# Kernel optimization log

Measured on AMD Instinct MI355X. Metric: run time of the kernel, lower is better.

The kernel has to match this reference:

```python
import jax, jax.numpy as jnp
import numpy as np

N = 50000            # nodes (cells)
E_RAND = 1_600_000   # random edges; self loops appended -> E = E_RAND + N
DIMS = [(512, 384), (384, 256), (256, 128)]  # (in, hidden) per encoder stage
OUT = 128


def setup_inputs() -> dict:
    key = jax.random.key(0)
    ks = jax.random.split(key, 16)
    features = jax.random.normal(ks[0], (N, DIMS[0][0]), dtype=jnp.float32)
    src = jax.random.randint(ks[1], (E_RAND,), 0, N, dtype=jnp.int32)
    dst = jax.random.randint(ks[2], (E_RAND,), 0, N, dtype=jnp.int32)
    loops = jnp.arange(N, dtype=jnp.int32)  # dgl.add_self_loop
    src = jnp.concatenate([src, loops])
    dst = jnp.concatenate([dst, loops])
    inp = {"features": features, "src": src, "dst": dst}
    i = 3
    for s, (din, dout) in enumerate(DIMS):
        inp[f"sage_w{s}"] = jax.random.normal(ks[i], (dout, din), jnp.float32) / np.sqrt(din); i += 1
        inp[f"sage_b{s}"] = jnp.zeros((dout,), jnp.float32)
        inp[f"gc_w{s}"] = jax.random.normal(ks[i], (dout, dout), jnp.float32) / np.sqrt(dout); i += 1
        inp[f"gc_b{s}"] = jnp.zeros((dout,), jnp.float32)
    inp["fc_w"] = jax.random.normal(ks[i], (OUT, DIMS[-1][1]), jnp.float32) / np.sqrt(DIMS[-1][1])
    inp["fc_b"] = jnp.zeros((OUT,), jnp.float32)
    return inp


def reference(features, src, dst,
              sage_w0, sage_b0, gc_w0, gc_b0,
              sage_w1, sage_b1, gc_w1, gc_b1,
              sage_w2, sage_b2, gc_w2, gc_b2,
              fc_w, fc_b):
    ones = jnp.ones((src.shape[0],), jnp.float32)
    in_deg = jax.ops.segment_sum(ones, dst, num_segments=N)
    out_deg = jax.ops.segment_sum(ones, src, num_segments=N)
    # GraphConv norm='both' scalers (clamp degree to >=1, as DGL does)
    inv_src = jnp.where(out_deg > 0, out_deg, 1.0) ** -0.5  # [N]
    inv_dst = jnp.where(in_deg > 0, in_deg, 1.0) ** -0.5    # [N]
    sage_den = (in_deg + 1.0)[:, None]                      # SAGE 'gcn' denominator

    def sage_gcn(h, w, b):
        # DGL SAGEConv aggregator_type='gcn': (sum_neigh + self)/(in_deg+1) -> fc_neigh
        agg = jax.ops.segment_sum(h[src], dst, num_segments=N)
        return ((agg + h) / sage_den) @ w.T + b

    def graph_conv(h, w, b):
        # DGL GraphConv norm='both': D_out^{-1/2} -> sum aggregate -> D_in^{-1/2} -> W
        hn = h * inv_src[:, None]
        agg = jax.ops.segment_sum(hn[src], dst, num_segments=N)
        return (agg * inv_dst[:, None]) @ w.T + b

    params = [(sage_w0, sage_b0, gc_w0, gc_b0),
              (sage_w1, sage_b1, gc_w1, gc_b1),
              (sage_w2, sage_b2, gc_w2, gc_b2)]
    h = features
    for sw, sb, gw, gb in params:
        h = jax.nn.relu(sage_gcn(h, sw, sb))
        h = jax.nn.relu(graph_conv(h, gw, gb))
    return h @ fc_w.T + fc_b
```

## Files before the change

kernel.cpp:

```cpp
#include <hip/hip_runtime.h>
#include <cstddef>
#include <cstdint>


typedef _Float16 h8 __attribute__((ext_vector_type(8)));
typedef _Float16 h4 __attribute__((ext_vector_type(4)));
typedef float f32x4 __attribute__((ext_vector_type(4)));

#define HB 64
#define NCH 256


__global__ __launch_bounds__(1024) void histo_dst_kernel(
    const int* __restrict__ dst, uint32_t* __restrict__ H,
    int* __restrict__ ord, int E, int bins2, int CE) {
  __shared__ uint32_t hh[25088];
  for (int i = threadIdx.x; i < bins2; i += 1024) hh[i] = 0;
  __syncthreads();
  const int base = blockIdx.x * CE;
  int lim = base + CE; if (lim > E) lim = E;
  for (int e = base + (int)threadIdx.x; e < lim; e += 1024) {
    int d = dst[e];
    const int sh = (d & 1) * 16;
    uint32_t old = atomicAdd(&hh[d >> 1], 1u << sh);
    ord[e] = (int)((old >> sh) & 0xFFFFu);
  }
  __syncthreads();
  uint32_t* out = H + (size_t)blockIdx.x * bins2;
  for (int i = threadIdx.x; i < bins2; i += 1024) out[i] = hh[i];
}

__global__ __launch_bounds__(1024) void histo_out_kernel(
    const int* __restrict__ src, uint32_t* __restrict__ H, int E, int bins2) {
  __shared__ uint32_t hh[25088];
  for (int i = threadIdx.x; i < bins2; i += 1024) hh[i] = 0;
  __syncthreads();
  const int C = (E + HB - 1) / HB;
  const int base = blockIdx.x * C;
  int lim = base + C; if (lim > E) lim = E;
  for (int e = base + (int)threadIdx.x; e < lim; e += 1024) {
    int s = src[e];
    atomicAdd(&hh[s >> 1], 1u << ((s & 1) * 16));
  }
  __syncthreads();
  uint32_t* out = H + (size_t)blockIdx.x * bins2;
  for (int i = threadIdx.x; i < bins2; i += 1024) out[i] = hh[i];
}

__global__ __launch_bounds__(256) void chunk_scan_kernel(
    uint32_t* __restrict__ Hd, const uint32_t* __restrict__ Hs,
    int* __restrict__ in_deg, int* __restrict__ out_deg, int bins2, int n) {
  int i = blockIdx.x * 256 + threadIdx.x;
  if (i >= bins2) return;
  uint32_t lo = 0, hi = 0;
  for (int c = 0; c < NCH; ++c) {
    uint32_t* p = Hd + (size_t)c * bins2 + i;
    uint32_t v = *p;
    *p = lo | (hi << 16);
    lo += v & 0xFFFFu;
    hi += v >> 16;
  }
  in_deg[2 * i] = (int)lo;
  if (2 * i + 1 < n) in_deg[2 * i + 1] = (int)hi;
  uint32_t slo = 0, shi = 0;
  for (int b = 0; b < HB; ++b) {
    uint32_t v = Hs[(size_t)b * bins2 + i];
    slo += v & 0xFFFFu;
    shi += v >> 16;
  }
  out_deg[2 * i] = (int)slo;
  if (2 * i + 1 < n) out_deg[2 * i + 1] = (int)shi;
}


__global__ __launch_bounds__(256) void scan_a(
    const int* __restrict__ deg, int* __restrict__ bsum, int n) {
  __shared__ int s[256];
  int i = blockIdx.x * 256 + threadIdx.x;
  s[threadIdx.x] = (i < n) ? deg[i] : 0;
  __syncthreads();
  #pragma unroll
  for (int off = 128; off > 0; off >>= 1) {
    if ((int)threadIdx.x < off) s[threadIdx.x] += s[threadIdx.x + off];
    __syncthreads();
  }
  if (threadIdx.x == 0) bsum[blockIdx.x] = s[0];
}

__global__ __launch_bounds__(256) void scan_b(
    int* __restrict__ bsum, int* __restrict__ rp, int nb, int n) {
  __shared__ int s[256];
  const int t = threadIdx.x;
  int v = (t < nb) ? bsum[t] : 0;
  s[t] = v;
  __syncthreads();
  #pragma unroll
  for (int off = 1; off < 256; off <<= 1) {
    int a = (t >= off) ? s[t - off] : 0;
    __syncthreads();
    s[t] += a;
    __syncthreads();
  }
  bsum[256 + t] = s[t] - v;
  if (t == 255) rp[n] = s[255];
}

__global__ __launch_bounds__(256) void scan_c(
    const int* __restrict__ in_deg, const int* __restrict__ out_deg,
    const int* __restrict__ bsum, int* __restrict__ rp,
    float* __restrict__ inv_src, float* __restrict__ inv_dst,
    float* __restrict__ inv_den, int n) {
  __shared__ int s[256];
  const int t = threadIdx.x;
  const int i = blockIdx.x * 256 + t;
  int v = (i < n) ? in_deg[i] : 0;
  s[t] = v;
  __syncthreads();
  #pragma unroll
  for (int off = 1; off < 256; off <<= 1) {
    int a = (t >= off) ? s[t - off] : 0;
    __syncthreads();
    s[t] += a;
    __syncthreads();
  }
  if (i < n) {
    rp[i] = bsum[256 + blockIdx.x] + s[t] - v;
    float od = (float)out_deg[i];
    float id = (float)v;
    inv_src[i] = rsqrtf(od > 0.f ? od : 1.0f);
    inv_dst[i] = rsqrtf(id > 0.f ? id : 1.0f);
    inv_den[i] = 1.0f / (id + 1.0f);
  }
}

__global__ __launch_bounds__(1024) void scatter_kernel(
    const int* __restrict__ src, const int* __restrict__ dst,
    const int* __restrict__ rp, const int* __restrict__ ord,
    const uint32_t* __restrict__ H, int* __restrict__ csr,
    int E, int bins2, int CE) {
  __shared__ uint32_t hh[25088];
  const uint32_t* Hc = H + (size_t)blockIdx.x * bins2;
  for (int i = threadIdx.x; i < bins2; i += 1024) hh[i] = Hc[i];
  __syncthreads();
  const int base = blockIdx.x * CE;
  int lim = base + CE; if (lim > E) lim = E;
  for (int e = base + (int)threadIdx.x; e < lim; e += 1024) {
    int d = dst[e];
    int b = (int)((hh[d >> 1] >> ((d & 1) * 16)) & 0xFFFFu);
    csr[rp[d] + b + ord[e]] = src[e];
  }
}


__global__ __launch_bounds__(256) void cvt_kernel(
    const float* __restrict__ in, _Float16* __restrict__ out,
    long n_in, long n_pad) {
  long i = ((long)blockIdx.x * 256 + (long)threadIdx.x) * 4;
  if (i >= n_pad) return;
  float4 v = (i < n_in) ? *(const float4*)(in + i) : make_float4(0.f, 0.f, 0.f, 0.f);
  h4 h = {(_Float16)v.x, (_Float16)v.y, (_Float16)v.z, (_Float16)v.w};
  *(h4*)(out + i) = h;
}

struct WArgs {
  const float* s[7];
  _Float16* d[7];
  int n[7];
};

__global__ __launch_bounds__(256) void wcvt_kernel(WArgs a) {
  const int w = blockIdx.y;
  long i = ((long)blockIdx.x * 256 + (long)threadIdx.x) * 4;
  if (i >= a.n[w]) return;
  float4 v = *(const float4*)(a.s[w] + i);
  h4 h = {(_Float16)v.x, (_Float16)v.y, (_Float16)v.z, (_Float16)v.w};
  *(h4*)(a.d[w] + i) = h;
}


__device__ __forceinline__ void gload_lds16(const _Float16* g, _Float16* l) {
  __builtin_amdgcn_global_load_lds(
      (const __attribute__((address_space(1))) void*)g,
      (__attribute__((address_space(3))) void*)l, 16, 0, 0);
}


template <typename OutT>
__global__ __launch_bounds__(256) void hgemm(
    const _Float16* __restrict__ A, const _Float16* __restrict__ W,
    OutT* __restrict__ C, int Mstore, int K, int Nc,
    const float* __restrict__ row_scale, const float* __restrict__ bias) {
  __shared__ _Float16 As[2][128 * 32];
  __shared__ _Float16 Bs[2][128 * 32];
  const int tid = threadIdx.x;
  const int bm = blockIdx.x * 128, bn = blockIdx.y * 128;
  const int wave = tid >> 6, lane = tid & 63;
  const int wm = (wave & 1) * 64, wn = (wave >> 1) * 64;
  const int lrow = lane & 15, lq = lane >> 4;

  const int r0 = tid >> 2;
  const int cc = (tid & 3) * 8;
  const _Float16* Ag = A + (size_t)(bm + r0) * K + cc;
  const _Float16* Wg = W + (size_t)(bn + r0) * K + cc;
  const size_t rs64 = (size_t)64 * K;
  const int l8 = tid * 8;

  f32x4 acc[4][4];
  #pragma unroll
  for (int i = 0; i < 4; ++i)
    #pragma unroll
    for (int j = 0; j < 4; ++j) acc[i][j] = (f32x4){0.f, 0.f, 0.f, 0.f};

  const int nt = K >> 5;
  gload_lds16(Ag, As[0] + l8);
  gload_lds16(Ag + rs64, As[0] + 64 * 32 + l8);
  gload_lds16(Wg, Bs[0] + l8);
  gload_lds16(Wg + rs64, Bs[0] + 64 * 32 + l8);
  __syncthreads();

  int cur = 0;
  for (int t = 0; t < nt; ++t) {
    if (t + 1 < nt) {
      const int k1 = (t + 1) << 5;
      gload_lds16(Ag + k1, As[cur ^ 1] + l8);
      gload_lds16(Ag + rs64 + k1, As[cur ^ 1] + 64 * 32 + l8);
      gload_lds16(Wg + k1, Bs[cur ^ 1] + l8);
      gload_lds16(Wg + rs64 + k1, Bs[cur ^ 1] + 64 * 32 + l8);
    }
    h8 af[4], bf[4];
    #pragma unroll
    for (int i = 0; i < 4; ++i)
      af[i] = *(const h8*)(As[cur] + (wm + i * 16 + lrow) * 32 + lq * 8);
    #pragma unroll
    for (int j = 0; j < 4; ++j)
      bf[j] = *(const h8*)(Bs[cur] + (wn + j * 16 + lrow) * 32 + lq * 8);
    #pragma unroll
    for (int i = 0; i < 4; ++i)
      #pragma unroll
      for (int j = 0; j < 4; ++j)
        acc[i][j] = __builtin_amdgcn_mfma_f32_16x16x32_f16(af[i], bf[j], acc[i][j], 0, 0, 0);
    __syncthreads();
    cur ^= 1;
  }

  #pragma unroll
  for (int i = 0; i < 4; ++i) {
    #pragma unroll
    for (int r = 0; r < 4; ++r) {
      const int m = bm + wm + i * 16 + lq * 4 + r;
      if (m < Mstore) {
        const float rsc = row_scale ? row_scale[m] : 1.0f;
        OutT* crow = C + (size_t)m * Nc + bn + wn + lrow;
        #pragma unroll
        for (int j = 0; j < 4; ++j) {
          float v = acc[i][j][r] * rsc;
          if (bias) v += bias[bn + wn + j * 16 + lrow];
          crow[j * 16] = (OutT)v;
        }
      }
    }
  }
}


template <int D, bool SELF>
__global__ __launch_bounds__(256) void agg_h(
    const _Float16* __restrict__ Z, const int* __restrict__ row_ptr,
    const int* __restrict__ csr, const float* __restrict__ out_scale,
    const float* __restrict__ bias, _Float16* __restrict__ out, int n) {
  constexpr int CH = D / 8;
  constexpr int GROUP = 16;
  constexpr int NV = CH / GROUP;
  const int gid = threadIdx.x >> 4;
  const int lane = threadIdx.x & 15;
  const int stride = gridDim.x * 16;

  for (int node = blockIdx.x * 16 + gid; node < n; node += stride) {
    const int rs = row_ptr[node], re = row_ptr[node + 1];

    float acc[NV][8];
    #pragma unroll
    for (int v = 0; v < NV; ++v)
      #pragma unroll
      for (int q = 0; q < 8; ++q) acc[v][q] = 0.f;

    for (int e = rs; e < re; e += GROUP) {
      int m = re - e; if (m > GROUP) m = GROUP;
      int eid = (lane < m) ? csr[e + lane] : 0;
      for (int j = 0; j < m; ++j) {
        int s = __shfl(eid, j, GROUP);
        const h8* zr = (const h8*)(Z + (size_t)s * D);
        #pragma unroll
        for (int v = 0; v < NV; ++v) {
          h8 t = zr[lane + v * GROUP];
          #pragma unroll
          for (int q = 0; q < 8; ++q) acc[v][q] += (float)t[q];
        }
      }
    }

    const float osc = out_scale[node];
    const h8* zs = (const h8*)(Z + (size_t)node * D);
    _Float16* orow = out + (size_t)node * D;
    #pragma unroll
    for (int v = 0; v < NV; ++v) {
      const int idx = lane + v * GROUP;
      if (SELF) {
        h8 t = zs[idx];
        #pragma unroll
        for (int q = 0; q < 8; ++q) acc[v][q] += (float)t[q];
      }
      h8 r;
      #pragma unroll
      for (int q = 0; q < 8; ++q) {
        float x = acc[v][q] * osc + bias[idx * 8 + q];
        r[q] = (_Float16)fmaxf(x, 0.f);
      }
      *(h8*)(orow + idx * 8) = r;
    }
  }
}


extern "C" void kernel_launch(void* const* d_in, const int* in_sizes, int n_in,
                              void* d_out, int out_size, void* d_ws, size_t ws_size,
                              hipStream_t stream) {
  const float* features = (const float*)d_in[0];
  const int*   src      = (const int*)d_in[1];
  const int*   dst      = (const int*)d_in[2];
  const float* wsrc[7] = {(const float*)d_in[3],  (const float*)d_in[5],
                          (const float*)d_in[7],  (const float*)d_in[9],
                          (const float*)d_in[11], (const float*)d_in[13],
                          (const float*)d_in[15]};
  const float* sb[3] = {(const float*)d_in[4],  (const float*)d_in[8],  (const float*)d_in[12]};
  const float* gb[3] = {(const float*)d_in[6],  (const float*)d_in[10], (const float*)d_in[14]};
  const float* fc_b  = (const float*)d_in[16];

  const int N = in_sizes[0] / 512;
  const int E = in_sizes[1];
  const int MB = (N + 127) / 128;
  const int Mpad = MB * 128;
  const int bins2 = (N + 1) / 2;
  if (bins2 > 25088) return;

  const int wcnt[7] = {384 * 512, 384 * 384, 256 * 384, 256 * 256,
                       128 * 256, 128 * 128, 128 * 128};

  char* ws = (char*)d_ws;
  _Float16* featH = (_Float16*)ws;
  _Float16* hA    = featH + (size_t)Mpad * 512;
  _Float16* hB    = hA + (size_t)Mpad * 384;
  _Float16* wH[7];
  {
    _Float16* p = hB + (size_t)Mpad * 384;
    for (int i = 0; i < 7; ++i) { wH[i] = p; p += wcnt[i]; }
  }
  int* csr     = (int*)(wH[6] + wcnt[6]);
  int* rp      = csr + E;
  int* in_dg   = rp + (N + 1);
  int* out_dg  = in_dg + N;
  int* sblk    = out_dg + N;
  float* inv_src = (float*)(sblk + N);
  float* inv_dst = inv_src + N;
  float* inv_den = inv_dst + N;

  int*      ord  = (int*)hB;
  uint32_t* Hsrc = (uint32_t*)(ord + E);
  uint32_t* Hdst = (uint32_t*)hA;

  size_t totw = 0; for (int i = 0; i < 7; ++i) totw += wcnt[i];
  size_t needed = ((size_t)Mpad * (512 + 384 + 384) + totw) * 2 +
                  ((size_t)E + (N + 1) + 6 * (size_t)N) * 4;
  if (ws_size < needed) return;

  const int CE = (E + NCH - 1) / NCH;
  const int nb256 = (N + 255) / 256;
  const int binsb = (bins2 + 255) / 256;

  histo_dst_kernel<<<NCH, 1024, 0, stream>>>(dst, Hdst, ord, E, bins2, CE);
  histo_out_kernel<<<HB, 1024, 0, stream>>>(src, Hsrc, E, bins2);
  chunk_scan_kernel<<<binsb, 256, 0, stream>>>(Hdst, Hsrc, in_dg, out_dg, bins2, N);
  scan_a<<<nb256, 256, 0, stream>>>(in_dg, sblk, N);
  scan_b<<<1, 256, 0, stream>>>(sblk, rp, nb256, N);
  scan_c<<<nb256, 256, 0, stream>>>(in_dg, out_dg, sblk, rp,
                                    inv_src, inv_dst, inv_den, N);
  scatter_kernel<<<NCH, 1024, 0, stream>>>(src, dst, rp, ord, Hdst, csr,
                                           E, bins2, CE);

  {
    long thr = (long)Mpad * 512 / 4;
    cvt_kernel<<<(int)((thr + 255) / 256), 256, 0, stream>>>(
        features, featH, (long)N * 512, (long)Mpad * 512);
    WArgs wa;
    int maxn = 0;
    for (int i = 0; i < 7; ++i) {
      wa.s[i] = wsrc[i]; wa.d[i] = wH[i]; wa.n[i] = wcnt[i];
      if (wcnt[i] > maxn) maxn = wcnt[i];
    }
    dim3 wg((maxn / 4 + 255) / 256, 7);
    wcvt_kernel<<<wg, 256, 0, stream>>>(wa);
  }

  const int dout[3] = {384, 256, 128};
  const _Float16* h = featH;
  int K = 512;
  const int ab = (N + 31) / 32;
  for (int s = 0; s < 3; ++s) {
    const int D = dout[s];
    dim3 gg(MB, D / 128);
    hgemm<_Float16><<<gg, 256, 0, stream>>>(h, wH[2 * s], hB, Mpad, K, D, nullptr, nullptr);
    if (D == 384)      agg_h<384, true><<<ab, 256, 0, stream>>>(hB, rp, csr, inv_den, sb[s], hA, N);
    else if (D == 256) agg_h<256, true><<<ab, 256, 0, stream>>>(hB, rp, csr, inv_den, sb[s], hA, N);
    else               agg_h<128, true><<<ab, 256, 0, stream>>>(hB, rp, csr, inv_den, sb[s], hA, N);
    hgemm<_Float16><<<gg, 256, 0, stream>>>(hA, wH[2 * s + 1], hB, Mpad, D, D, inv_src, nullptr);
    if (D == 384)      agg_h<384, false><<<ab, 256, 0, stream>>>(hB, rp, csr, inv_dst, gb[s], hA, N);
    else if (D == 256) agg_h<256, false><<<ab, 256, 0, stream>>>(hB, rp, csr, inv_dst, gb[s], hA, N);
    else               agg_h<128, false><<<ab, 256, 0, stream>>>(hB, rp, csr, inv_dst, gb[s], hA, N);
    h = hA;
    K = D;
  }
  dim3 gf(MB, 1);
  hgemm<float><<<gf, 256, 0, stream>>>(h, wH[6], (float*)d_out, N, 128, 128, nullptr, fc_b);
}
```

Baseline: 1.171 ms.

## Store GEMM output in column panels and aggregate per panel for cache locality

```diff
diff --git a/kernel.cpp b/kernel.cpp
--- a/kernel.cpp
+++ b/kernel.cpp
@@ -189,7 +189,8 @@
 __global__ __launch_bounds__(256) void hgemm(
     const _Float16* __restrict__ A, const _Float16* __restrict__ W,
     OutT* __restrict__ C, int Mstore, int K, int Nc,
-    const float* __restrict__ row_scale, const float* __restrict__ bias) {
+    const float* __restrict__ row_scale, const float* __restrict__ bias,
+    int pw) {
   __shared__ _Float16 As[2][128 * 32];
   __shared__ _Float16 Bs[2][128 * 32];
   const int tid = threadIdx.x;
@@ -250,12 +251,15 @@
       const int m = bm + wm + i * 16 + lq * 4 + r;
       if (m < Mstore) {
         const float rsc = row_scale ? row_scale[m] : 1.0f;
-        OutT* crow = C + (size_t)m * Nc + bn + wn + lrow;
         #pragma unroll
         for (int j = 0; j < 4; ++j) {
+          const int c = bn + wn + j * 16 + lrow;
           float v = acc[i][j][r] * rsc;
-          if (bias) v += bias[bn + wn + j * 16 + lrow];
-          crow[j * 16] = (OutT)v;
+          if (bias) v += bias[c];
+          const size_t off = pw
+              ? ((size_t)(c / pw) * (size_t)Mstore * pw + (size_t)m * pw + (c % pw))
+              : ((size_t)m * Nc + (size_t)c);
+          C[off] = (OutT)v;
         }
       }
     }
@@ -263,60 +267,57 @@
 }
 
 
-template <int D, bool SELF>
-__global__ __launch_bounds__(256) void agg_h(
-    const _Float16* __restrict__ Z, const int* __restrict__ row_ptr,
+template <int W, int NPAN, bool SELF>
+__global__ __launch_bounds__(256) void agg_p(
+    const _Float16* __restrict__ Zpm, const int* __restrict__ row_ptr,
     const int* __restrict__ csr, const float* __restrict__ out_scale,
-    const float* __restrict__ bias, _Float16* __restrict__ out, int n) {
-  constexpr int CH = D / 8;
-  constexpr int GROUP = 16;
-  constexpr int NV = CH / GROUP;
-  const int gid = threadIdx.x >> 4;
-  const int lane = threadIdx.x & 15;
-  const int stride = gridDim.x * 16;
-
-  for (int node = blockIdx.x * 16 + gid; node < n; node += stride) {
+    const float* __restrict__ bias, _Float16* __restrict__ out,
+    int n, int Mpad, int D, int T) {
+  constexpr int ACT = W / 8;
+  constexpr int REP = 8 / NPAN;
+  const int pslot = blockIdx.x & 7;
+  const int panel = pslot % NPAN;
+  const int rep   = pslot / NPAN;
+  const int tix   = (blockIdx.x >> 3) * REP + rep;
+  const int ntile = T * REP;
+  const int gid   = threadIdx.x >> 3;
+  const int l8    = threadIdx.x & 7;
+  const _Float16* Zp = Zpm + (size_t)panel * ((size_t)Mpad * W);
+  const int cbase = panel * W + l8 * 8;
+
+  for (int node = tix * 32 + gid; node < n; node += ntile * 32) {
     const int rs = row_ptr[node], re = row_ptr[node + 1];
-
-    float acc[NV][8];
-    #pragma unroll
-    for (int v = 0; v < NV; ++v)
-      #pragma unroll
-      for (int q = 0; q < 8; ++q) acc[v][q] = 0.f;
-
-    for (int e = rs; e < re; e += GROUP) {
-      int m = re - e; if (m > GROUP) m = GROUP;
-      int eid = (lane < m) ? csr[e + lane] : 0;
+    float acc[8];
+    #pragma unroll
+    for (int q = 0; q < 8; ++q) acc[q] = 0.f;
+
+    for (int e = rs; e < re; e += 8) {
+      int m = re - e; if (m > 8) m = 8;
+      int eid = (l8 < m) ? __builtin_nontemporal_load(csr + e + l8) : 0;
       for (int j = 0; j < m; ++j) {
-        int s = __shfl(eid, j, GROUP);
-        const h8* zr = (const h8*)(Z + (size_t)s * D);
-        #pragma unroll
-        for (int v = 0; v < NV; ++v) {
-          h8 t = zr[lane + v * GROUP];
+        int s = __shfl(eid, j, 8);
+        if (l8 < ACT) {
+          h8 t = *(const h8*)(Zp + (size_t)s * W + l8 * 8);
           #pragma unroll
-          for (int q = 0; q < 8; ++q) acc[v][q] += (float)t[q];
+          for (int q = 0; q < 8; ++q) acc[q] += (float)t[q];
         }
       }
     }
 
-    const float osc = out_scale[node];
-    const h8* zs = (const h8*)(Z + (size_t)node * D);
-    _Float16* orow = out + (size_t)node * D;
-    #pragma unroll
-    for (int v = 0; v < NV; ++v) {
-      const int idx = lane + v * GROUP;
+    if (l8 < ACT) {
       if (SELF) {
-        h8 t = zs[idx];
+        h8 t = *(const h8*)(Zp + (size_t)node * W + l8 * 8);
         #pragma unroll
-        for (int q = 0; q < 8; ++q) acc[v][q] += (float)t[q];
+        for (int q = 0; q < 8; ++q) acc[q] += (float)t[q];
       }
+      const float osc = out_scale[node];
       h8 r;
       #pragma unroll
       for (int q = 0; q < 8; ++q) {
-        float x = acc[v][q] * osc + bias[idx * 8 + q];
+        float x = acc[q] * osc + bias[cbase + q];
         r[q] = (_Float16)fmaxf(x, 0.f);
       }
-      *(h8*)(orow + idx * 8) = r;
+      __builtin_nontemporal_store(r, (h8*)(out + (size_t)node * D + cbase));
     }
   }
 }
@@ -402,23 +403,29 @@
   }
 
   const int dout[3] = {384, 256, 128};
+  const int pwj[3]  = {48, 32, 32};
   const _Float16* h = featH;
   int K = 512;
-  const int ab = (N + 31) / 32;
+  const int T = 192;
+  const int ag = 8 * T;
   for (int s = 0; s < 3; ++s) {
     const int D = dout[s];
+    const int pw = pwj[s];
     dim3 gg(MB, D / 128);
-    hgemm<_Float16><<<gg, 256, 0, stream>>>(h, wH[2 * s], hB, Mpad, K, D, nullptr, nullptr);
-    if (D == 384)      agg_h<384, true><<<ab, 256, 0, stream>>>(hB, rp, csr, inv_den, sb[s], hA, N);
-    else if (D == 256) agg_h<256, true><<<ab, 256, 0, stream>>>(hB, rp, csr, inv_den, sb[s], hA, N);
-    else               agg_h<128, true><<<ab, 256, 0, stream>>>(hB, rp, csr, inv_den, sb[s], hA, N);
-    hgemm<_Float16><<<gg, 256, 0, stream>>>(hA, wH[2 * s + 1], hB, Mpad, D, D, inv_src, nullptr);
-    if (D == 384)      agg_h<384, false><<<ab, 256, 0, stream>>>(hB, rp, csr, inv_dst, gb[s], hA, N);
-    else if (D == 256) agg_h<256, false><<<ab, 256, 0, stream>>>(hB, rp, csr, inv_dst, gb[s], hA, N);
-    else               agg_h<128, false><<<ab, 256, 0, stream>>>(hB, rp, csr, inv_dst, gb[s], hA, N);
+    hgemm<_Float16><<<gg, 256, 0, stream>>>(h, wH[2 * s], hB, Mpad, K, D,
+                                            nullptr, nullptr, pw);
+    if (D == 384)      agg_p<48, 8, true><<<ag, 256, 0, stream>>>(hB, rp, csr, inv_den, sb[s], hA, N, Mpad, D, T);
+    else if (D == 256) agg_p<32, 8, true><<<ag, 256, 0, stream>>>(hB, rp, csr, inv_den, sb[s], hA, N, Mpad, D, T);
+    else               agg_p<32, 4, true><<<ag, 256, 0, stream>>>(hB, rp, csr, inv_den, sb[s], hA, N, Mpad, D, T);
+    hgemm<_Float16><<<gg, 256, 0, stream>>>(hA, wH[2 * s + 1], hB, Mpad, D, D,
+                                            inv_src, nullptr, pw);
+    if (D == 384)      agg_p<48, 8, false><<<ag, 256, 0, stream>>>(hB, rp, csr, inv_dst, gb[s], hA, N, Mpad, D, T);
+    else if (D == 256) agg_p<32, 8, false><<<ag, 256, 0, stream>>>(hB, rp, csr, inv_dst, gb[s], hA, N, Mpad, D, T);
+    else               agg_p<32, 4, false><<<ag, 256, 0, stream>>>(hB, rp, csr, inv_dst, gb[s], hA, N, Mpad, D, T);
     h = hA;
     K = D;
   }
   dim3 gf(MB, 1);
-  hgemm<float><<<gf, 256, 0, stream>>>(h, wH[6], (float*)d_out, N, 128, 128, nullptr, fc_b);
-}
+  hgemm<float><<<gf, 256, 0, stream>>>(h, wH[6], (float*)d_out, N, 128, 128,
+                                       nullptr, fc_b, 0);
+}
```

Result: slower. 1.653 ms (+41.1%).
